# Performance work log

Hardware: AMD Instinct MI355X
Metric: run time of the kernel (lower is better)

## Reference

```python
import jax, jax.numpy as jnp
import numpy as np

GROUPS = 32
EPS = 1e-5
HEAD_DIM = 64


def group_norm(x, gamma, beta):
    # x: [B, L, C]; normalize over (L, C//G) within each of G channel groups
    B, L, C = x.shape
    g = x.reshape(B, L, GROUPS, C // GROUPS)
    mean = g.mean(axis=(1, 3), keepdims=True)
    var = g.var(axis=(1, 3), keepdims=True)
    g = (g - mean) * jax.lax.rsqrt(var + EPS)
    return g.reshape(B, L, C) * gamma + beta


def setup_inputs() -> dict:
    key = jax.random.key(0)
    ks = jax.random.split(key, 4)
    B, H, W, C = 16, 32, 32, 512
    x = jax.random.normal(ks[0], (B, H, W, C), dtype=jnp.float32)
    timesteps = jax.random.randint(ks[1], (B,), 0, 1000)
    gamma = jnp.ones((C,), jnp.float32)
    beta = jnp.zeros((C,), jnp.float32)
    w_qkv = jax.random.normal(ks[2], (C, 3 * C), dtype=jnp.float32) * (1.0 / np.sqrt(C))
    b_qkv = jnp.zeros((3 * C,), jnp.float32)
    w_out = jax.random.normal(ks[3], (C, C), dtype=jnp.float32) * (1.0 / np.sqrt(C))
    b_out = jnp.zeros((C,), jnp.float32)
    return {"x": x, "timesteps": timesteps, "gamma": gamma, "beta": beta,
            "w_qkv": w_qkv, "b_qkv": b_qkv, "w_out": w_out, "b_out": b_out}


def reference(x, timesteps, gamma, beta, w_qkv, b_qkv, w_out, b_out):
    B, H, W, C = x.shape
    L = H * W
    nh = C // HEAD_DIM
    factor = jnp.asarray(1.0 / np.sqrt(np.sqrt(HEAD_DIM)), x.dtype)  # applied to both q and k

    xf = x.reshape(B, L, C)
    qkv = group_norm(xf, gamma, beta) @ w_qkv + b_qkv        # [B, L, 3C]
    q, k, v = jnp.split(qkv, 3, axis=-1)

    def heads(t):  # [B, L, C] -> [B, nh, L, d]
        return t.reshape(B, L, nh, HEAD_DIM).transpose(0, 2, 1, 3)

    q, k, v = heads(q) * factor, heads(k) * factor, heads(v)
    scores = jnp.einsum('bhqd,bhkd->bhqk', q, k)             # [B, nh, L, L]
    attn = jax.nn.softmax(scores, axis=-1)
    out = jnp.einsum('bhqk,bhkd->bhqd', attn, v)             # [B, nh, L, d]
    out = out.transpose(0, 2, 1, 3).reshape(B, L, C)
    h = out @ w_out + b_out
    return (xf + h).reshape(B, H, W, C)
```

## Files before the change

kernel.cpp:

```cpp
#include <hip/hip_runtime.h>

#define Bn 16
#define Ln 1024
#define Cn 512
#define Mn (Bn*Ln)
#define N3n 1536

typedef unsigned short u16;
typedef __attribute__((ext_vector_type(8))) short short8;
typedef __attribute__((ext_vector_type(4))) float f32x4;

typedef const __attribute__((address_space(1))) void* gas_p;
typedef __attribute__((address_space(3))) void* las_p;

__device__ inline void gl_lds16(const void* g, void* l) {
  __builtin_amdgcn_global_load_lds((gas_p)g, (las_p)l, 16, 0, 0);
}

__device__ inline u16 f2bf(float f) {
  union { float f; unsigned u; } v; v.f = f;
  unsigned r = v.u + 0x7FFFu + ((v.u >> 16) & 1u);
  return (u16)(r >> 16);
}

__device__ inline f32x4 mfma16(short8 a, short8 b, f32x4 c) {
  return __builtin_amdgcn_mfma_f32_16x16x32_bf16(a, b, c, 0, 0, 0);
}

__global__ __launch_bounds__(256) void k_gn(const float* __restrict__ x,
                                            const float* __restrict__ gamma,
                                            const float* __restrict__ beta,
                                            u16* __restrict__ gn) {
  __shared__ __attribute__((aligned(16))) float xs[1024 * 32];
  __shared__ float red[32];
  __shared__ float stat[4];
  int bid = blockIdx.x;
  int b = bid >> 4, gp = bid & 15;
  const float* base = x + (size_t)b * (Ln * Cn) + gp * 32;
  int tid = threadIdx.x;
  int c = tid & 7;
  float s1 = 0.f, s2 = 0.f;
  for (int i = 0; i < 32; ++i) {
    int s = i * 256 + tid;
    int r = s >> 3;
    float4 v = *(const float4*)(base + (size_t)r * Cn + c * 4);
    *(float4*)(xs + (size_t)s * 4) = v;
    s1 += v.x + v.y + v.z + v.w;
    s2 += v.x * v.x + v.y * v.y + v.z * v.z + v.w * v.w;
  }
  s1 += __shfl_xor(s1, 1);  s2 += __shfl_xor(s2, 1);
  s1 += __shfl_xor(s1, 2);  s2 += __shfl_xor(s2, 2);
  s1 += __shfl_xor(s1, 8);  s2 += __shfl_xor(s2, 8);
  s1 += __shfl_xor(s1, 16); s2 += __shfl_xor(s2, 16);
  s1 += __shfl_xor(s1, 32); s2 += __shfl_xor(s2, 32);
  int w = tid >> 6, lane = tid & 63;
  if (lane == 0) { red[w * 2 + 0] = s1; red[16 + w * 2 + 0] = s2; }
  if (lane == 4) { red[w * 2 + 1] = s1; red[16 + w * 2 + 1] = s2; }
  __syncthreads();
  if (tid < 2) {
    float a = red[tid] + red[2 + tid] + red[4 + tid] + red[6 + tid];
    float q = red[16 + tid] + red[18 + tid] + red[20 + tid] + red[22 + tid];
    float mean = a * (1.f / 16384.f);
    float var = q * (1.f / 16384.f) - mean * mean;
    stat[tid * 2] = mean;
    stat[tid * 2 + 1] = rsqrtf(var + 1e-5f);
  }
  __syncthreads();
  float mean = stat[(c >> 2) * 2], rstd = stat[(c >> 2) * 2 + 1];
  float4 gv = *(const float4*)(gamma + gp * 32 + c * 4);
  float4 bv = *(const float4*)(beta + gp * 32 + c * 4);
  u16* gdst = gn + (size_t)b * (Ln * Cn) + gp * 32;
  for (int i = 0; i < 32; ++i) {
    int s = i * 256 + tid;
    int r = s >> 3;
    float4 v = *(const float4*)(xs + (size_t)s * 4);
    ushort4 o;
    o.x = f2bf((v.x - mean) * rstd * gv.x + bv.x);
    o.y = f2bf((v.y - mean) * rstd * gv.y + bv.y);
    o.z = f2bf((v.z - mean) * rstd * gv.z + bv.z);
    o.w = f2bf((v.w - mean) * rstd * gv.w + bv.w);
    *(ushort4*)(gdst + (size_t)r * Cn + c * 4) = o;
  }
}

__global__ __launch_bounds__(256) void k_wtrans(const float* __restrict__ wqkv,
                                                const float* __restrict__ wout,
                                                u16* __restrict__ wqkvT,
                                                u16* __restrict__ woutT) {
  int id = blockIdx.x * 256 + threadIdx.x;
  if (id < Cn * N3n) {
    int k = id & 511, n = id >> 9;
    wqkvT[id] = f2bf(wqkv[(size_t)k * N3n + n]);
  } else {
    int id2 = id - Cn * N3n;
    int k = id2 & 511, n = id2 >> 9;
    woutT[id2] = f2bf(wout[(size_t)k * Cn + n]);
  }
}

__global__ __launch_bounds__(256) void k_qkv(const u16* __restrict__ gn,
                                             const u16* __restrict__ wT,
                                             const float* __restrict__ bias,
                                             u16* __restrict__ qb,
                                             u16* __restrict__ kb,
                                             u16* __restrict__ vT) {
  __shared__ __attribute__((aligned(16))) char smem[66560];
  int bid = blockIdx.x;
  int wg = (bid & 7) * 192 + (bid >> 3);
  int tn = wg % 12, tm = wg / 12;
  int m0 = tm * 128, n0 = tn * 128;
  int tid = threadIdx.x;
  int w = tid >> 6, lane = tid & 63, lr = lane & 15, lg = lane >> 4;
  int wr = w >> 1, wc = w & 1;
  const f32x4 fzero = {0.f, 0.f, 0.f, 0.f};
  f32x4 acc[4][4];
#pragma unroll
  for (int mi = 0; mi < 4; ++mi)
#pragma unroll
    for (int ni = 0; ni < 4; ++ni) acc[mi][ni] = fzero;

#pragma unroll
  for (int i = 0; i < 4; ++i) {
    int s = i * 256 + tid;
    int r = s >> 3, c = s & 7;
    gl_lds16(gn + ((size_t)(m0 + r) * 512 + ((c ^ (r & 7)) << 3)),
             smem + ((s & ~63) << 4));
    gl_lds16(wT + ((size_t)(n0 + r) * 512 + ((c ^ (r & 7)) << 3)),
             smem + 32768 + ((s & ~63) << 4));
  }
  __syncthreads();

  for (int kt = 0; kt < 8; ++kt) {
    int cur = kt & 1;
    char* Asb = smem + cur * 16384;
    char* Bsb = smem + 32768 + cur * 16384;
    if (kt < 7) {
      int nb = cur ^ 1, k0n = (kt + 1) * 64;
#pragma unroll
      for (int i = 0; i < 4; ++i) {
        int s = i * 256 + tid;
        int r = s >> 3, c = s & 7;
        gl_lds16(gn + ((size_t)(m0 + r) * 512 + k0n + ((c ^ (r & 7)) << 3)),
                 smem + nb * 16384 + ((s & ~63) << 4));
        gl_lds16(wT + ((size_t)(n0 + r) * 512 + k0n + ((c ^ (r & 7)) << 3)),
                 smem + 32768 + nb * 16384 + ((s & ~63) << 4));
      }
    }
#pragma unroll
    for (int ks = 0; ks < 2; ++ks) {
      short8 af[4], bf[4];
#pragma unroll
      for (int mi = 0; mi < 4; ++mi) {
        int row = wr * 64 + mi * 16 + lr;
        int ck = ks * 4 + lg;
        af[mi] = *(const short8*)(Asb + row * 128 + ((ck ^ (lr & 7)) << 4));
      }
#pragma unroll
      for (int ni = 0; ni < 4; ++ni) {
        int row = wc * 64 + ni * 16 + lr;
        int ck = ks * 4 + lg;
        bf[ni] = *(const short8*)(Bsb + row * 128 + ((ck ^ (lr & 7)) << 4));
      }
#pragma unroll
      for (int mi = 0; mi < 4; ++mi)
#pragma unroll
        for (int ni = 0; ni < 4; ++ni)
          acc[mi][ni] = mfma16(af[mi], bf[ni], acc[mi][ni]);
    }
    __syncthreads();
  }

  if (tn >= 8) {
    float* T = (float*)smem;
#pragma unroll
    for (int mi = 0; mi < 4; ++mi)
#pragma unroll
      for (int ni = 0; ni < 4; ++ni) {
        int n_l = wc * 64 + ni * 16 + lr;
        float bn = bias[n0 + n_l];
#pragma unroll
        for (int rr = 0; rr < 4; ++rr) {
          int m_l = wr * 64 + mi * 16 + lg * 4 + rr;
          T[n_l * 130 + m_l] = acc[mi][ni][rr] + bn;
        }
      }
    __syncthreads();
    int n_l = tid >> 1, half = tid & 1;
    int nv = n0 - 1024 + n_l;
    int h = nv >> 6, dd = nv & 63;
    int bb = m0 >> 10, li0 = m0 & 1023;
    u16* dst = vT + ((size_t)(bb * 8 + h) * 64 + dd) * 1024 + li0;
    const float* Tr = T + n_l * 130;
#pragma unroll
    for (int j = 0; j < 8; ++j) {
      int mb = half * 8 + 16 * j;
      uint4 o;
      o.x = (unsigned)f2bf(Tr[mb + 0]) | ((unsigned)f2bf(Tr[mb + 1]) << 16);
      o.y = (unsigned)f2bf(Tr[mb + 2]) | ((unsigned)f2bf(Tr[mb + 3]) << 16);
      o.z = (unsigned)f2bf(Tr[mb + 4]) | ((unsigned)f2bf(Tr[mb + 5]) << 16);
      o.w = (unsigned)f2bf(Tr[mb + 6]) | ((unsigned)f2bf(Tr[mb + 7]) << 16);
      *(uint4*)(dst + mb) = o;
    }
  } else {
#pragma unroll
    for (int mi = 0; mi < 4; ++mi) {
#pragma unroll
      for (int ni = 0; ni < 4; ++ni) {
        int n = n0 + wc * 64 + ni * 16 + lr;
        float bn = bias[n];
        int which = n >> 9, nn = n & 511;
        int h = nn >> 6, dd = nn & 63;
#pragma unroll
        for (int rr = 0; rr < 4; ++rr) {
          int m = m0 + wr * 64 + mi * 16 + lg * 4 + rr;
          float v = acc[mi][ni][rr] + bn;
          int bb = m >> 10, li = m & 1023;
          if (which == 0)
            qb[((size_t)(bb * 8 + h) * 1024 + li) * 64 + dd] = f2bf(v);
          else
            kb[((size_t)(bb * 8 + h) * 1024 + li) * 64 + dd] = f2bf(v);
        }
      }
    }
  }
}

__global__ __launch_bounds__(512, 4) void k_attn(const u16* __restrict__ qb,
                                                 const u16* __restrict__ kb,
                                                 const u16* __restrict__ vT,
                                                 u16* __restrict__ ob) {
  __shared__ __attribute__((aligned(16))) u16 Ks[3 * 64 * 64];
  __shared__ __attribute__((aligned(16))) u16 Vs[3 * 64 * 64];
  __shared__ __attribute__((aligned(16))) u16 Ps[8 * 32 * 64];
  int bid = blockIdx.x;
  int xq = bid & 7, kk = bid >> 3;
  int bh = ((kk & 15) << 3) | xq;
  int qt = kk >> 4;
  const u16* qh = qb + (size_t)bh * 65536;
  const u16* kh = kb + (size_t)bh * 65536;
  const u16* vh = vT + (size_t)bh * 65536;
  int tid = threadIdx.x, w = tid >> 6, lane = tid & 63, lr = lane & 15, lg = lane >> 4;
  int q0 = qt * 256 + w * 32;
  const f32x4 fzero = {0.f, 0.f, 0.f, 0.f};
  const float C1 = 0.18033688011112042f;

  short8 qf[2][2];
#pragma unroll
  for (int mi = 0; mi < 2; ++mi)
#pragma unroll
    for (int ks = 0; ks < 2; ++ks)
      qf[mi][ks] = *(const short8*)(qh + (size_t)(q0 + mi * 16 + lr) * 64 +
                                    ks * 32 + lg * 8);
  f32x4 accO[2][4];
  float mst[2], lst[2], nmc[2];
#pragma unroll
  for (int mi = 0; mi < 2; ++mi) {
#pragma unroll
    for (int nd = 0; nd < 4; ++nd) accO[mi][nd] = fzero;
    mst[mi] = -1e30f; lst[mi] = 0.f; nmc[mi] = 0.f;
  }
  char* Pwb = (char*)(Ps + w * 2048);

  int sr = tid >> 3, sc8 = tid & 7;
  size_t koff = (size_t)sr * 64 + ((sc8 ^ (sr & 7)) << 3);
  size_t voff = (size_t)sr * 1024 + ((sc8 ^ (sr & 7)) << 3);
  int ldst = (tid & ~63) << 4;

  gl_lds16(kh + koff, (char*)Ks + ldst);
  gl_lds16(vh + voff, (char*)Vs + ldst);
  gl_lds16(kh + 4096 + koff, (char*)Ks + 8192 + ldst);
  gl_lds16(vh + 64 + voff, (char*)Vs + 8192 + ldst);
  asm volatile("s_waitcnt vmcnt(2)" ::: "memory");
  __builtin_amdgcn_s_barrier();

#pragma unroll 1
  for (int jt = 0; jt < 16; ++jt) {
    int cb = jt % 3;
    char* Ksb = (char*)Ks + cb * 8192;
    char* Vsb = (char*)Vs + cb * 8192;
    if (jt < 14) {
      int nb = (jt + 2) % 3;
      gl_lds16(kh + (size_t)(jt + 2) * 4096 + koff, (char*)Ks + nb * 8192 + ldst);
      gl_lds16(vh + (size_t)(jt + 2) * 64 + voff, (char*)Vs + nb * 8192 + ldst);
    }

    short8 kf[4][2];
#pragma unroll
    for (int nj = 0; nj < 4; ++nj)
#pragma unroll
      for (int ks = 0; ks < 2; ++ks) {
        int row = nj * 16 + lr;
        kf[nj][ks] = *(const short8*)(Ksb + row * 128 + (((ks * 4 + lg) ^ (row & 7)) << 4));
      }

    f32x4 sc[2][4];
#pragma unroll
    for (int mi = 0; mi < 2; ++mi)
#pragma unroll
      for (int nj = 0; nj < 4; ++nj) sc[mi][nj] = fzero;
#pragma unroll
    for (int ks = 0; ks < 2; ++ks)
#pragma unroll
      for (int mi = 0; mi < 2; ++mi)
#pragma unroll
        for (int nj = 0; nj < 4; ++nj)
          sc[mi][nj] = mfma16(kf[nj][ks], qf[mi][ks], sc[mi][nj]);

#pragma unroll
    for (int mi = 0; mi < 2; ++mi) {
      float t0 = fmaxf(fmaxf(sc[mi][0][0], sc[mi][0][1]), fmaxf(sc[mi][0][2], sc[mi][0][3]));
      float t1 = fmaxf(fmaxf(sc[mi][1][0], sc[mi][1][1]), fmaxf(sc[mi][1][2], sc[mi][1][3]));
      float t2 = fmaxf(fmaxf(sc[mi][2][0], sc[mi][2][1]), fmaxf(sc[mi][2][2], sc[mi][2][3]));
      float t3 = fmaxf(fmaxf(sc[mi][3][0], sc[mi][3][1]), fmaxf(sc[mi][3][2], sc[mi][3][3]));
      float mloc = fmaxf(fmaxf(t0, t1), fmaxf(t2, t3));
      mloc = fmaxf(mloc, __shfl_xor(mloc, 16));
      mloc = fmaxf(mloc, __shfl_xor(mloc, 32));
      if (__any(mloc - mst[mi] > 8.f)) {
        float mn = fmaxf(mst[mi], mloc);
        float al = __builtin_amdgcn_exp2f((mst[mi] - mn) * C1);
        mst[mi] = mn;
        nmc[mi] = -mn * C1;
        lst[mi] *= al;
#pragma unroll
        for (int rr = 0; rr < 4; ++rr) {
          float ab = __shfl(al, (lane & 48) | ((lane >> 4) & 3) * 4 + rr);
#pragma unroll
          for (int nd = 0; nd < 4; ++nd) accO[mi][nd][rr] *= ab;
        }
      }
      float nm = nmc[mi];
      float rs = 0.f;
#pragma unroll
      for (int nj = 0; nj < 4; ++nj) {
        float p0 = __builtin_amdgcn_exp2f(__builtin_fmaf(sc[mi][nj][0], C1, nm));
        float p1 = __builtin_amdgcn_exp2f(__builtin_fmaf(sc[mi][nj][1], C1, nm));
        float p2 = __builtin_amdgcn_exp2f(__builtin_fmaf(sc[mi][nj][2], C1, nm));
        float p3 = __builtin_amdgcn_exp2f(__builtin_fmaf(sc[mi][nj][3], C1, nm));
        rs += (p0 + p1) + (p2 + p3);
        unsigned u0 = __float_as_uint(p0), u1 = __float_as_uint(p1);
        unsigned u2 = __float_as_uint(p2), u3 = __float_as_uint(p3);
        uint2 pv;
        pv.x = (u0 >> 16) | (u1 & 0xFFFF0000u);
        pv.y = (u2 >> 16) | (u3 & 0xFFFF0000u);
        int row = mi * 16 + lr;
        int byte = row * 128 + (nj * 16 + lg * 4) * 2;
        byte ^= (row & 7) << 4;
        *(uint2*)(Pwb + byte) = pv;
      }
      lst[mi] += rs;
    }

    short8 bv[4][2];
#pragma unroll
    for (int nd = 0; nd < 4; ++nd)
#pragma unroll
      for (int ks = 0; ks < 2; ++ks) {
        int row = nd * 16 + lr;
        bv[nd][ks] = *(const short8*)(Vsb + row * 128 + (((ks * 4 + lg) ^ (row & 7)) << 4));
      }

    short8 ap[2][2];
#pragma unroll
    for (int mi = 0; mi < 2; ++mi)
#pragma unroll
      for (int ks = 0; ks < 2; ++ks) {
        int row = mi * 16 + lr;
        int byte = row * 128 + (ks * 32 + lg * 8) * 2;
        byte ^= (row & 7) << 4;
        ap[mi][ks] = *(const short8*)(Pwb + byte);
      }
#pragma unroll
    for (int ks = 0; ks < 2; ++ks)
#pragma unroll
      for (int mi = 0; mi < 2; ++mi)
#pragma unroll
        for (int nd = 0; nd < 4; ++nd)
          accO[mi][nd] = mfma16(ap[mi][ks], bv[nd][ks], accO[mi][nd]);

    if (jt < 14)
      asm volatile("s_waitcnt vmcnt(2)" ::: "memory");
    else
      asm volatile("s_waitcnt vmcnt(0)" ::: "memory");
    __builtin_amdgcn_s_barrier();
  }

  int b = bh >> 3, h = bh & 7;
#pragma unroll
  for (int mi = 0; mi < 2; ++mi) {
    float lt = lst[mi];
    lt += __shfl_xor(lt, 16);
    lt += __shfl_xor(lt, 32);
    float il = 1.f / lt;
#pragma unroll
    for (int rr = 0; rr < 4; ++rr) {
      float ib = __shfl(il, (lane & 48) | ((lane >> 4) & 3) * 4 + rr);
      int row = q0 + mi * 16 + lg * 4 + rr;
#pragma unroll
      for (int nd = 0; nd < 4; ++nd) {
        int col = h * 64 + nd * 16 + lr;
        ob[(size_t)(b * 1024 + row) * 512 + col] = f2bf(accO[mi][nd][rr] * ib);
      }
    }
  }
}

__global__ __launch_bounds__(256) void k_out(const u16* __restrict__ ob,
                                             const u16* __restrict__ wT,
                                             const float* __restrict__ bias,
                                             const float* __restrict__ x,
                                             float* __restrict__ out) {
  __shared__ __attribute__((aligned(16))) u16 As[2 * 128 * 64];
  __shared__ __attribute__((aligned(16))) u16 Bs[2 * 128 * 64];
  int bid = blockIdx.x;
  int wg = (bid & 7) * 64 + (bid >> 3);
  int tn = wg & 3, tm = wg >> 2;
  int m0 = tm * 128, n0 = tn * 128;
  int tid = threadIdx.x;
  int w = tid >> 6, lane = tid & 63, lr = lane & 15, lg = lane >> 4;
  int wr = w >> 1, wc = w & 1;
  const f32x4 fzero = {0.f, 0.f, 0.f, 0.f};
  f32x4 acc[4][4];
#pragma unroll
  for (int mi = 0; mi < 4; ++mi)
#pragma unroll
    for (int ni = 0; ni < 4; ++ni) acc[mi][ni] = fzero;

#pragma unroll
  for (int i = 0; i < 4; ++i) {
    int s = i * 256 + tid;
    int r = s >> 3, c = s & 7;
    gl_lds16(ob + ((size_t)(m0 + r) * 512 + ((c ^ (r & 7)) << 3)),
             (char*)As + ((s & ~63) << 4));
    gl_lds16(wT + ((size_t)(n0 + r) * 512 + ((c ^ (r & 7)) << 3)),
             (char*)Bs + ((s & ~63) << 4));
  }
  __syncthreads();

  for (int kt = 0; kt < 8; ++kt) {
    int cur = kt & 1;
    char* Asb = (char*)As + cur * 16384;
    char* Bsb = (char*)Bs + cur * 16384;
    if (kt < 7) {
      int nb = cur ^ 1, k0n = (kt + 1) * 64;
#pragma unroll
      for (int i = 0; i < 4; ++i) {
        int s = i * 256 + tid;
        int r = s >> 3, c = s & 7;
        gl_lds16(ob + ((size_t)(m0 + r) * 512 + k0n + ((c ^ (r & 7)) << 3)),
                 (char*)As + nb * 16384 + ((s & ~63) << 4));
        gl_lds16(wT + ((size_t)(n0 + r) * 512 + k0n + ((c ^ (r & 7)) << 3)),
                 (char*)Bs + nb * 16384 + ((s & ~63) << 4));
      }
    }
#pragma unroll
    for (int ks = 0; ks < 2; ++ks) {
      short8 af[4], bf[4];
#pragma unroll
      for (int mi = 0; mi < 4; ++mi) {
        int row = wr * 64 + mi * 16 + lr;
        int ck = ks * 4 + lg;
        af[mi] = *(const short8*)(Asb + row * 128 + ((ck ^ (lr & 7)) << 4));
      }
#pragma unroll
      for (int ni = 0; ni < 4; ++ni) {
        int row = wc * 64 + ni * 16 + lr;
        int ck = ks * 4 + lg;
        bf[ni] = *(const short8*)(Bsb + row * 128 + ((ck ^ (lr & 7)) << 4));
      }
#pragma unroll
      for (int mi = 0; mi < 4; ++mi)
#pragma unroll
        for (int ni = 0; ni < 4; ++ni)
          acc[mi][ni] = mfma16(af[mi], bf[ni], acc[mi][ni]);
    }
    __syncthreads();
  }
#pragma unroll
  for (int mi = 0; mi < 4; ++mi) {
#pragma unroll
    for (int ni = 0; ni < 4; ++ni) {
      int n = n0 + wc * 64 + ni * 16 + lr;
      float bn = bias[n];
#pragma unroll
      for (int rr = 0; rr < 4; ++rr) {
        int m = m0 + wr * 64 + mi * 16 + lg * 4 + rr;
        size_t off = (size_t)m * 512 + n;
        out[off] = x[off] + acc[mi][ni][rr] + bn;
      }
    }
  }
}

extern "C" void kernel_launch(void* const* d_in, const int* in_sizes, int n_in,
                              void* d_out, int out_size, void* d_ws, size_t ws_size,
                              hipStream_t stream) {
  const float* x = (const float*)d_in[0];
  const float* gamma = (const float*)d_in[2];
  const float* beta = (const float*)d_in[3];
  const float* wqkv = (const float*)d_in[4];
  const float* bqkv = (const float*)d_in[5];
  const float* wout = (const float*)d_in[6];
  const float* bout = (const float*)d_in[7];
  float* out = (float*)d_out;

  char* ws = (char*)d_ws;
  u16* gn = (u16*)(ws + 4096);
  u16* wqkvT = (u16*)(ws + 4096 + 16777216);
  u16* woutT = (u16*)(ws + 4096 + 16777216 + 1572864);
  u16* qb = (u16*)(ws + 4096 + 16777216 + 1572864 + 524288);
  u16* kb = qb + 8388608;
  u16* vT = kb + 8388608;
  u16* ob = vT + 8388608;

  k_gn<<<256, 256, 0, stream>>>(x, gamma, beta, gn);
  k_wtrans<<<4096, 256, 0, stream>>>(wqkv, wout, wqkvT, woutT);
  k_qkv<<<1536, 256, 0, stream>>>(gn, wqkvT, bqkv, qb, kb, vT);
  k_attn<<<512, 512, 0, stream>>>(qb, kb, vT, ob);
  k_out<<<512, 256, 0, stream>>>(ob, woutT, bout, x, out);
}
```

Measured before the change: 139.8 us.

## Switch attention to 32x32x16 MFMA and keep P in registers

```diff
diff --git a/kernel.cpp b/kernel.cpp
--- a/kernel.cpp
+++ b/kernel.cpp
@@ -9,6 +9,7 @@
 typedef unsigned short u16;
 typedef __attribute__((ext_vector_type(8))) short short8;
 typedef __attribute__((ext_vector_type(4))) float f32x4;
+typedef __attribute__((ext_vector_type(16))) float f32x16;
 
 typedef const __attribute__((address_space(1))) void* gas_p;
 typedef __attribute__((address_space(3))) void* las_p;
@@ -23,8 +24,15 @@
   return (u16)(r >> 16);
 }
 
+__device__ inline unsigned pk2(float a, float b) {
+  return (__float_as_uint(a) >> 16) | (__float_as_uint(b) & 0xFFFF0000u);
+}
+
 __device__ inline f32x4 mfma16(short8 a, short8 b, f32x4 c) {
   return __builtin_amdgcn_mfma_f32_16x16x32_bf16(a, b, c, 0, 0, 0);
+}
+__device__ inline f32x16 mfma32(short8 a, short8 b, f32x16 c) {
+  return __builtin_amdgcn_mfma_f32_32x32x16_bf16(a, b, c, 0, 0, 0);
 }
 
 __global__ __launch_bounds__(256) void k_gn(const float* __restrict__ x,
@@ -231,7 +239,6 @@
                                                  u16* __restrict__ ob) {
   __shared__ __attribute__((aligned(16))) u16 Ks[3 * 64 * 64];
   __shared__ __attribute__((aligned(16))) u16 Vs[3 * 64 * 64];
-  __shared__ __attribute__((aligned(16))) u16 Ps[8 * 32 * 64];
   int bid = blockIdx.x;
   int xq = bid & 7, kk = bid >> 3;
   int bh = ((kk & 15) << 3) | xq;
@@ -239,27 +246,22 @@
   const u16* qh = qb + (size_t)bh * 65536;
   const u16* kh = kb + (size_t)bh * 65536;
   const u16* vh = vT + (size_t)bh * 65536;
-  int tid = threadIdx.x, w = tid >> 6, lane = tid & 63, lr = lane & 15, lg = lane >> 4;
+  int tid = threadIdx.x, w = tid >> 6, lane = tid & 63;
+  int l31 = lane & 31, lhi = lane >> 5;
   int q0 = qt * 256 + w * 32;
-  const f32x4 fzero = {0.f, 0.f, 0.f, 0.f};
   const float C1 = 0.18033688011112042f;
 
-  short8 qf[2][2];
-#pragma unroll
-  for (int mi = 0; mi < 2; ++mi)
-#pragma unroll
-    for (int ks = 0; ks < 2; ++ks)
-      qf[mi][ks] = *(const short8*)(qh + (size_t)(q0 + mi * 16 + lr) * 64 +
-                                    ks * 32 + lg * 8);
-  f32x4 accO[2][4];
-  float mst[2], lst[2], nmc[2];
-#pragma unroll
-  for (int mi = 0; mi < 2; ++mi) {
-#pragma unroll
-    for (int nd = 0; nd < 4; ++nd) accO[mi][nd] = fzero;
-    mst[mi] = -1e30f; lst[mi] = 0.f; nmc[mi] = 0.f;
-  }
-  char* Pwb = (char*)(Ps + w * 2048);
+  short8 qf[4];
+#pragma unroll
+  for (int ks = 0; ks < 4; ++ks)
+    qf[ks] = *(const short8*)(qh + (size_t)(q0 + l31) * 64 + ks * 16 + lhi * 8);
+
+  f32x16 accO[2];
+#pragma unroll
+  for (int dt = 0; dt < 2; ++dt)
+#pragma unroll
+    for (int r = 0; r < 16; ++r) accO[dt][r] = 0.f;
+  float mst = -1e30f, lst = 0.f, nmc = 0.f;
 
   int sr = tid >> 3, sc8 = tid & 7;
   size_t koff = (size_t)sr * 64 + ((sc8 ^ (sr & 7)) << 3);
@@ -284,98 +286,91 @@
       gl_lds16(vh + (size_t)(jt + 2) * 64 + voff, (char*)Vs + nb * 8192 + ldst);
     }
 
-    short8 kf[4][2];
-#pragma unroll
-    for (int nj = 0; nj < 4; ++nj)
-#pragma unroll
-      for (int ks = 0; ks < 2; ++ks) {
-        int row = nj * 16 + lr;
-        kf[nj][ks] = *(const short8*)(Ksb + row * 128 + (((ks * 4 + lg) ^ (row & 7)) << 4));
-      }
-
-    f32x4 sc[2][4];
-#pragma unroll
-    for (int mi = 0; mi < 2; ++mi)
-#pragma unroll
-      for (int nj = 0; nj < 4; ++nj) sc[mi][nj] = fzero;
-#pragma unroll
-    for (int ks = 0; ks < 2; ++ks)
-#pragma unroll
-      for (int mi = 0; mi < 2; ++mi)
-#pragma unroll
-        for (int nj = 0; nj < 4; ++nj)
-          sc[mi][nj] = mfma16(kf[nj][ks], qf[mi][ks], sc[mi][nj]);
-
-#pragma unroll
-    for (int mi = 0; mi < 2; ++mi) {
-      float t0 = fmaxf(fmaxf(sc[mi][0][0], sc[mi][0][1]), fmaxf(sc[mi][0][2], sc[mi][0][3]));
-      float t1 = fmaxf(fmaxf(sc[mi][1][0], sc[mi][1][1]), fmaxf(sc[mi][1][2], sc[mi][1][3]));
-      float t2 = fmaxf(fmaxf(sc[mi][2][0], sc[mi][2][1]), fmaxf(sc[mi][2][2], sc[mi][2][3]));
-      float t3 = fmaxf(fmaxf(sc[mi][3][0], sc[mi][3][1]), fmaxf(sc[mi][3][2], sc[mi][3][3]));
-      float mloc = fmaxf(fmaxf(t0, t1), fmaxf(t2, t3));
-      mloc = fmaxf(mloc, __shfl_xor(mloc, 16));
-      mloc = fmaxf(mloc, __shfl_xor(mloc, 32));
-      if (__any(mloc - mst[mi] > 8.f)) {
-        float mn = fmaxf(mst[mi], mloc);
-        float al = __builtin_amdgcn_exp2f((mst[mi] - mn) * C1);
-        mst[mi] = mn;
-        nmc[mi] = -mn * C1;
-        lst[mi] *= al;
-#pragma unroll
-        for (int rr = 0; rr < 4; ++rr) {
-          float ab = __shfl(al, (lane & 48) | ((lane >> 4) & 3) * 4 + rr);
-#pragma unroll
-          for (int nd = 0; nd < 4; ++nd) accO[mi][nd][rr] *= ab;
+    f32x16 sc0, sc1;
+#pragma unroll
+    for (int r = 0; r < 16; ++r) { sc0[r] = 0.f; sc1[r] = 0.f; }
+#pragma unroll
+    for (int ks = 0; ks < 4; ++ks) {
+      int row = l31;
+      short8 kf = *(const short8*)(Ksb + row * 128 + (((2 * ks + lhi) ^ (row & 7)) << 4));
+      sc0 = mfma32(kf, qf[ks], sc0);
+    }
+#pragma unroll
+    for (int ks = 0; ks < 4; ++ks) {
+      int row = 32 + l31;
+      short8 kf = *(const short8*)(Ksb + row * 128 + (((2 * ks + lhi) ^ (row & 7)) << 4));
+      sc1 = mfma32(kf, qf[ks], sc1);
+    }
+
+    float mloc = sc0[0];
+#pragma unroll
+    for (int r = 1; r < 16; ++r) mloc = fmaxf(mloc, sc0[r]);
+#pragma unroll
+    for (int r = 0; r < 16; ++r) mloc = fmaxf(mloc, sc1[r]);
+    mloc = fmaxf(mloc, __shfl_xor(mloc, 32));
+    if (__any(mloc - mst > 8.f)) {
+      float mn = fmaxf(mst, mloc);
+      float al = __builtin_amdgcn_exp2f((mst - mn) * C1);
+      mst = mn; nmc = -mn * C1; lst *= al;
+#pragma unroll
+      for (int reg = 0; reg < 16; ++reg) {
+        float ab = __shfl(al, (reg & 3) + 8 * (reg >> 2) + 4 * lhi);
+        accO[0][reg] *= ab;
+        accO[1][reg] *= ab;
+      }
+    }
+    float rs = 0.f;
+#pragma unroll
+    for (int r = 0; r < 16; ++r) {
+      float p = __builtin_amdgcn_exp2f(__builtin_fmaf(sc0[r], C1, nmc));
+      sc0[r] = p; rs += p;
+    }
+#pragma unroll
+    for (int r = 0; r < 16; ++r) {
+      float p = __builtin_amdgcn_exp2f(__builtin_fmaf(sc1[r], C1, nmc));
+      sc1[r] = p; rs += p;
+    }
+    lst += rs;
+
+    short8 ap[4];
+#pragma unroll
+    for (int kt2 = 0; kt2 < 2; ++kt2) {
+#pragma unroll
+      for (int hh = 0; hh < 2; ++hh) {
+        unsigned A0, A1, B0, B1;
+        if (kt2 == 0) {
+          A0 = pk2(sc0[8 * hh + 0], sc0[8 * hh + 1]);
+          A1 = pk2(sc0[8 * hh + 2], sc0[8 * hh + 3]);
+          B0 = pk2(sc0[8 * hh + 4], sc0[8 * hh + 5]);
+          B1 = pk2(sc0[8 * hh + 6], sc0[8 * hh + 7]);
+        } else {
+          A0 = pk2(sc1[8 * hh + 0], sc1[8 * hh + 1]);
+          A1 = pk2(sc1[8 * hh + 2], sc1[8 * hh + 3]);
+          B0 = pk2(sc1[8 * hh + 4], sc1[8 * hh + 5]);
+          B1 = pk2(sc1[8 * hh + 6], sc1[8 * hh + 7]);
         }
-      }
-      float nm = nmc[mi];
-      float rs = 0.f;
-#pragma unroll
-      for (int nj = 0; nj < 4; ++nj) {
-        float p0 = __builtin_amdgcn_exp2f(__builtin_fmaf(sc[mi][nj][0], C1, nm));
-        float p1 = __builtin_amdgcn_exp2f(__builtin_fmaf(sc[mi][nj][1], C1, nm));
-        float p2 = __builtin_amdgcn_exp2f(__builtin_fmaf(sc[mi][nj][2], C1, nm));
-        float p3 = __builtin_amdgcn_exp2f(__builtin_fmaf(sc[mi][nj][3], C1, nm));
-        rs += (p0 + p1) + (p2 + p3);
-        unsigned u0 = __float_as_uint(p0), u1 = __float_as_uint(p1);
-        unsigned u2 = __float_as_uint(p2), u3 = __float_as_uint(p3);
-        uint2 pv;
-        pv.x = (u0 >> 16) | (u1 & 0xFFFF0000u);
-        pv.y = (u2 >> 16) | (u3 & 0xFFFF0000u);
-        int row = mi * 16 + lr;
-        int byte = row * 128 + (nj * 16 + lg * 4) * 2;
-        byte ^= (row & 7) << 4;
-        *(uint2*)(Pwb + byte) = pv;
-      }
-      lst[mi] += rs;
-    }
-
-    short8 bv[4][2];
-#pragma unroll
-    for (int nd = 0; nd < 4; ++nd)
-#pragma unroll
-      for (int ks = 0; ks < 2; ++ks) {
-        int row = nd * 16 + lr;
-        bv[nd][ks] = *(const short8*)(Vsb + row * 128 + (((ks * 4 + lg) ^ (row & 7)) << 4));
-      }
-
-    short8 ap[2][2];
-#pragma unroll
-    for (int mi = 0; mi < 2; ++mi)
-#pragma unroll
-      for (int ks = 0; ks < 2; ++ks) {
-        int row = mi * 16 + lr;
-        int byte = row * 128 + (ks * 32 + lg * 8) * 2;
-        byte ^= (row & 7) << 4;
-        ap[mi][ks] = *(const short8*)(Pwb + byte);
-      }
-#pragma unroll
-    for (int ks = 0; ks < 2; ++ks)
-#pragma unroll
-      for (int mi = 0; mi < 2; ++mi)
-#pragma unroll
-        for (int nd = 0; nd < 4; ++nd)
-          accO[mi][nd] = mfma16(ap[mi][ks], bv[nd][ks], accO[mi][nd]);
+        unsigned t0 = lhi ? A0 : B0;
+        unsigned t1 = lhi ? A1 : B1;
+        unsigned xt0 = __shfl_xor(t0, 32);
+        unsigned xt1 = __shfl_xor(t1, 32);
+        union { uint4 u; short8 s; } cv;
+        cv.u.x = lhi ? xt0 : A0;
+        cv.u.y = lhi ? xt1 : A1;
+        cv.u.z = lhi ? B0 : xt0;
+        cv.u.w = lhi ? B1 : xt1;
+        ap[2 * kt2 + hh] = cv.s;
+      }
+    }
+
+#pragma unroll
+    for (int ks2 = 0; ks2 < 4; ++ks2) {
+#pragma unroll
+      for (int dt = 0; dt < 2; ++dt) {
+        int row = dt * 32 + l31;
+        short8 bv = *(const short8*)(Vsb + row * 128 + (((2 * ks2 + lhi) ^ (row & 7)) << 4));
+        accO[dt] = mfma32(ap[ks2], bv, accO[dt]);
+      }
+    }
 
     if (jt < 14)
       asm volatile("s_waitcnt vmcnt(2)" ::: "memory");
@@ -385,21 +380,17 @@
   }
 
   int b = bh >> 3, h = bh & 7;
-#pragma unroll
-  for (int mi = 0; mi < 2; ++mi) {
-    float lt = lst[mi];
-    lt += __shfl_xor(lt, 16);
-    lt += __shfl_xor(lt, 32);
-    float il = 1.f / lt;
-#pragma unroll
-    for (int rr = 0; rr < 4; ++rr) {
-      float ib = __shfl(il, (lane & 48) | ((lane >> 4) & 3) * 4 + rr);
-      int row = q0 + mi * 16 + lg * 4 + rr;
-#pragma unroll
-      for (int nd = 0; nd < 4; ++nd) {
-        int col = h * 64 + nd * 16 + lr;
-        ob[(size_t)(b * 1024 + row) * 512 + col] = f2bf(accO[mi][nd][rr] * ib);
-      }
+  float lt = lst + __shfl_xor(lst, 32);
+  float il = 1.f / lt;
+#pragma unroll
+  for (int reg = 0; reg < 16; ++reg) {
+    int qrow = (reg & 3) + 8 * (reg >> 2) + 4 * lhi;
+    float ib = __shfl(il, qrow);
+    int row = q0 + qrow;
+#pragma unroll
+    for (int dt = 0; dt < 2; ++dt) {
+      int col = h * 64 + dt * 32 + l31;
+      ob[(size_t)(b * 1024 + row) * 512 + col] = f2bf(accO[dt][reg] * ib);
     }
   }
 }
```

Result: faster. 130.1 us (-6.9%).
